# Performance work log

Measured on AMD Instinct MI355X. Metric: run time of the kernel, lower is better.

## Reference

```python
import jax, jax.numpy as jnp
import numpy as np

DIM = 768


def setup_inputs() -> dict:
    key = jax.random.key(0)
    k1, k2, k3, k4, k5 = jax.random.split(key, 5)
    lines = jax.random.normal(k1, (32, 512, DIM), dtype=jnp.float32)
    videos = jax.random.normal(k2, (32, 128, DIM), dtype=jnp.float32)
    video_mask = jax.random.randint(k3, (32, 128), 0, 2, dtype=jnp.int32)
    # nn.Linear(dim, dim, bias=False) weights, applied as x @ W.T
    w_q = jax.random.normal(k4, (DIM, DIM), dtype=jnp.float32) * (DIM ** -0.5)
    w_k = jax.random.normal(k5, (DIM, DIM), dtype=jnp.float32) * (DIM ** -0.5)
    return {"lines": lines, "videos": videos, "video_mask": video_mask, "w_q": w_q, "w_k": w_k}


def reference(lines, videos, video_mask, w_q, w_k):
    scale = DIM ** -0.5
    q = jnp.einsum('bld,ed->ble', lines, w_q)   # (B, L, D)
    k = jnp.einsum('bvd,ed->bve', videos, w_k)  # (B, V, D)
    scores = jnp.einsum('bld,bvd->blv', q, k) * scale
    pad = (video_mask == 0)[:, None, :]          # (B, 1, V)
    scores = jnp.where(pad, jnp.float32(-1e9), scores)
    weights = jax.nn.softmax(scores, axis=-1)    # (B, L, V)
    return jnp.einsum('blv,bvd->bld', weights, videos)
```

## Files before the change

kernel.cpp:

```cpp
#include <hip/hip_runtime.h>

#define DIM 768
#define NB  32
#define LQ  512
#define NV  128

typedef unsigned short u16;
typedef unsigned int   u32;
typedef __bf16 bf16x8 __attribute__((ext_vector_type(8)));
typedef float  f32x4  __attribute__((ext_vector_type(4)));
typedef u16    u16x8  __attribute__((ext_vector_type(8)));
typedef u16    u16x4  __attribute__((ext_vector_type(4)));

typedef __attribute__((address_space(1))) const void gvoid;
typedef __attribute__((address_space(3))) void       svoid;

__device__ __forceinline__ u16 f2bf(float f) {
    u32 u = __float_as_uint(f);
    return (u16)((u + 0x7FFFu + ((u >> 16) & 1u)) >> 16);
}

__device__ __forceinline__ bf16x8 ld_frag(const u16* p) {
    return __builtin_bit_cast(bf16x8, *(const u16x8*)p);
}

__device__ __forceinline__ void gld16(const void* g, void* l) {
    __builtin_amdgcn_global_load_lds((gvoid*)g, (svoid*)l, 16, 0, 0);
}

#define W2S    4
#define W2_BLK (36 * W2S)
#define NL_BLK 6144

__global__ __launch_bounds__(256) void prep_kernel(const float* __restrict__ lines,
                                                   const float* __restrict__ w_q,
                                                   const float* __restrict__ w_k,
                                                   const float* __restrict__ videos,
                                                   u16* __restrict__ lbf,
                                                   float* __restrict__ w2f,
                                                   u16* __restrict__ vt2,
                                                   u16* __restrict__ vbf) {
    __shared__ union {
        u16 T[64][136];
        struct { u16 q[128][72]; u16 k[128][72]; } w2s;
    } uL;
    const int bx = blockIdx.x;
    const int t  = threadIdx.x;

    if (bx < W2_BLK) {
        const int tile = bx / W2S, kc = bx % W2S;
        const int m0 = (tile / 6) * 128;
        const int n0 = (tile % 6) * 128;
        const int w    = t >> 6;
        const int lane = t & 63;
        const int quad = lane >> 4;
        const int ln   = lane & 15;
        const int wr   = (w >> 1) * 64;
        const int wc   = (w & 1) * 64;
        f32x4 acc[4][4] = {};
        for (int ks = kc * 3; ks < kc * 3 + 3; ++ks) {
            __syncthreads();
            const int e0 = ks * 64;
#pragma unroll
            for (int p = 0; p < 8; ++p) {
                int f  = t + p * 256;
                int r  = f >> 5;
                int c4 = f & 31;
                float4 xq = *(const float4*)(w_q + (size_t)(e0 + r) * DIM + m0 + c4 * 4);
                float4 xk = *(const float4*)(w_k + (size_t)(e0 + r) * DIM + n0 + c4 * 4);
                int swz = ((r >> 3) ^ ((c4 >> 1) & 7)) * 8 + (r & 7);
                uL.w2s.q[c4 * 4 + 0][swz] = f2bf(xq.x);
                uL.w2s.q[c4 * 4 + 1][swz] = f2bf(xq.y);
                uL.w2s.q[c4 * 4 + 2][swz] = f2bf(xq.z);
                uL.w2s.q[c4 * 4 + 3][swz] = f2bf(xq.w);
                uL.w2s.k[c4 * 4 + 0][swz] = f2bf(xk.x);
                uL.w2s.k[c4 * 4 + 1][swz] = f2bf(xk.y);
                uL.w2s.k[c4 * 4 + 2][swz] = f2bf(xk.z);
                uL.w2s.k[c4 * 4 + 3][swz] = f2bf(xk.w);
            }
            __syncthreads();
#pragma unroll
            for (int kk = 0; kk < 2; ++kk) {
                bf16x8 af[4], bfr[4];
#pragma unroll
                for (int i = 0; i < 4; ++i) {
                    int row = wr + i * 16 + ln;
                    af[i]  = ld_frag(&uL.w2s.q[row][((kk * 4 + quad) ^ ((row >> 3) & 7)) * 8]);
                }
#pragma unroll
                for (int j = 0; j < 4; ++j) {
                    int row = wc + j * 16 + ln;
                    bfr[j] = ld_frag(&uL.w2s.k[row][((kk * 4 + quad) ^ ((row >> 3) & 7)) * 8]);
                }
#pragma unroll
                for (int i = 0; i < 4; ++i)
#pragma unroll
                    for (int j = 0; j < 4; ++j)
                        acc[i][j] = __builtin_amdgcn_mfma_f32_16x16x32_bf16(af[i], bfr[j], acc[i][j], 0, 0, 0);
            }
        }
#pragma unroll
        for (int i = 0; i < 4; ++i)
#pragma unroll
            for (int j = 0; j < 4; ++j)
#pragma unroll
                for (int r = 0; r < 4; ++r)
                    atomicAdd(&w2f[(size_t)(m0 + wr + i * 16 + quad * 4 + r) * DIM +
                                   n0 + wc + j * 16 + ln], acc[i][j][r]);
        return;
    }

    if (bx < W2_BLK + NL_BLK) {
        size_t i = (size_t)(bx - W2_BLK) * 256 + t;
        float4 a = ((const float4*)lines)[i * 2];
        float4 b = ((const float4*)lines)[i * 2 + 1];
        u16x8 o = { f2bf(a.x), f2bf(a.y), f2bf(a.z), f2bf(a.w),
                    f2bf(b.x), f2bf(b.y), f2bf(b.z), f2bf(b.w) };
        ((u16x8*)lbf)[i] = o;
        return;
    }

    const int v  = bx - (W2_BLK + NL_BLK);
    const int b  = v / 12;
    const int d0 = (v % 12) * 64;
    const float* src = videos + (size_t)b * NV * DIM;
#pragma unroll
    for (int p = 0; p < 8; ++p) {
        int f  = t + p * 256;
        int vv = f >> 4;
        int c4 = f & 15;
        float4 x = *(const float4*)(src + (size_t)vv * DIM + d0 + c4 * 4);
        u16x4 o = { f2bf(x.x), f2bf(x.y), f2bf(x.z), f2bf(x.w) };
        uL.T[c4 * 4 + 0][vv] = o[0];
        uL.T[c4 * 4 + 1][vv] = o[1];
        uL.T[c4 * 4 + 2][vv] = o[2];
        uL.T[c4 * 4 + 3][vv] = o[3];
        *(u16x4*)(vbf + ((size_t)b * NV + vv) * DIM + d0 + c4 * 4) = o;
    }
    __syncthreads();
#pragma unroll
    for (int p = 0; p < 4; ++p) {
        int f  = t + p * 256;
        int dl = f >> 4;
        int v8 = f & 15;
        int d  = d0 + dl;
        int it = d >> 7, wv = (d >> 4) & 7, lnn = d & 15;
        int ks = v8 >> 2, qd = v8 & 3;
        int lane = qd * 16 + lnn;
        size_t off = ((((size_t)b * 6 + it) * 8 + wv) * 4 + ks) * 512 + lane * 8;
        *(u16x8*)(vt2 + off) = *(const u16x8*)&uL.T[dl][v8 * 8];
    }
}

__global__ __launch_bounds__(512) void g_kernel(const u16* __restrict__ A,
                                                const float* __restrict__ Wf,
                                                u16* __restrict__ C) {
    __shared__ u16 sA[128][64];
    __shared__ u16 sB[128][72];
    const int t    = threadIdx.x;
    const int w    = t >> 6;
    const int lane = t & 63;
    const int quad = lane >> 4;
    const int ln   = lane & 15;

    int m0, n0;
    {
        int i = blockIdx.x;
        int xcd = i & 7, s = i >> 3;
        m0 = ((s / 6) * 8 + xcd) * 128;
        n0 = (s % 6) * 128;
    }

    const int wr = (w >> 2) * 64;
    const int wc = (w & 3) * 32;
    const int srow   = lane >> 3;
    const int schunk = (lane & 7) ^ srow;

    f32x4 acc[4][2] = {};
#pragma unroll
    for (int ks = 0; ks < 12; ++ks) {
        __syncthreads();
#pragma unroll
        for (int p = 0; p < 2; ++p) {
            int rb = w * 16 + p * 8;
            gld16(A + (size_t)(m0 + rb + srow) * DIM + ks * 64 + schunk * 8, &sA[rb][0]);
        }
#pragma unroll
        for (int p = 0; p < 4; ++p) {
            int idx = t + p * 512;
            int row = idx >> 4, c4 = idx & 15;
            float4 x = *(const float4*)(Wf + (size_t)(n0 + row) * DIM + ks * 64 + c4 * 4);
            u16x4 o = { f2bf(x.x), f2bf(x.y), f2bf(x.z), f2bf(x.w) };
            int swz = ((c4 >> 1) ^ (row & 7)) * 8 + (c4 & 1) * 4;
            *(u16x4*)&sB[row][swz] = o;
        }
        __syncthreads();
#pragma unroll
        for (int kk = 0; kk < 2; ++kk) {
            bf16x8 af[4], bfr[2];
#pragma unroll
            for (int i = 0; i < 4; ++i)
                af[i]  = ld_frag(&sA[wr + i * 16 + ln][((kk * 4 + quad) ^ (ln & 7)) * 8]);
#pragma unroll
            for (int j = 0; j < 2; ++j)
                bfr[j] = ld_frag(&sB[wc + j * 16 + ln][((kk * 4 + quad) ^ (ln & 7)) * 8]);
#pragma unroll
            for (int i = 0; i < 4; ++i)
#pragma unroll
                for (int j = 0; j < 2; ++j)
                    acc[i][j] = __builtin_amdgcn_mfma_f32_16x16x32_bf16(af[i], bfr[j], acc[i][j], 0, 0, 0);
        }
    }
#pragma unroll
    for (int i = 0; i < 4; ++i)
#pragma unroll
        for (int j = 0; j < 2; ++j)
#pragma unroll
            for (int r = 0; r < 4; ++r)
                C[(size_t)(m0 + wr + i * 16 + quad * 4 + r) * DIM + n0 + wc + j * 16 + ln] =
                    f2bf(acc[i][j][r]);
}

__global__ __launch_bounds__(512) void attn_kernel(const u16* __restrict__ Q,
                                                   const u16* __restrict__ K,
                                                   const u16* __restrict__ Vt2,
                                                   const int* __restrict__ mask,
                                                   float* __restrict__ out) {
    int b, l0;
    {
        int i = blockIdx.x;
        int xcd = i & 7, s = i >> 3;
        b  = (s >> 3) * 8 + xcd;
        l0 = (s & 7) * 64;
    }
    const int t    = threadIdx.x;
    const int w    = t >> 6;
    const int lane = t & 63;
    const int quad = lane >> 4;
    const int ln   = lane & 15;

    __shared__ union {
        struct { u16 q[64][64]; u16 k[128][64]; } st;
        float s[64][132];
    } uA;
    __shared__ union {
        struct { u16 q[64][64]; u16 k[128][64]; } st;
        u16 p[64][136];
    } uB;
    __shared__ float sBias[128];

    const u16* Qb = Q + ((size_t)b * LQ + l0) * DIM;
    const u16* Kb = K + (size_t)b * NV * DIM;
    if (t < NV) sBias[t] = mask[b * NV + t] ? 0.0f : -1e9f;

    const int srow   = lane >> 3;
    const int schunk = (lane & 7) ^ srow;

    auto stage = [&](int ks, int sel) {
        u16 (*q)[64] = sel ? uB.st.q : uA.st.q;
        u16 (*k)[64] = sel ? uB.st.k : uA.st.k;
        gld16(Qb + (size_t)(w * 8 + srow) * DIM + ks * 64 + schunk * 8, &q[w * 8][0]);
        gld16(Kb + (size_t)(w * 16 + srow) * DIM + ks * 64 + schunk * 8, &k[w * 16][0]);
        gld16(Kb + (size_t)(w * 16 + 8 + srow) * DIM + ks * 64 + schunk * 8, &k[w * 16 + 8][0]);
    };

    f32x4 accS[4] = {};
    stage(0, 0);
#pragma unroll
    for (int ks = 0; ks < 12; ++ks) {
        __syncthreads();
        if (ks < 11) stage(ks + 1, (ks + 1) & 1);
        u16 (*q)[64] = (ks & 1) ? uB.st.q : uA.st.q;
        u16 (*k)[64] = (ks & 1) ? uB.st.k : uA.st.k;
#pragma unroll
        for (int kk = 0; kk < 2; ++kk) {
            bf16x8 bfr = ld_frag(&k[w * 16 + ln][((kk * 4 + quad) ^ (ln & 7)) * 8]);
#pragma unroll
            for (int i = 0; i < 4; ++i) {
                bf16x8 af = ld_frag(&q[i * 16 + ln][((kk * 4 + quad) ^ (ln & 7)) * 8]);
                accS[i] = __builtin_amdgcn_mfma_f32_16x16x32_bf16(af, bfr, accS[i], 0, 0, 0);
            }
        }
    }
    __syncthreads();
    const float scale = 0.03608439182435161f;
#pragma unroll
    for (int i = 0; i < 4; ++i)
#pragma unroll
        for (int r = 0; r < 4; ++r)
            uA.s[i * 16 + quad * 4 + r][w * 16 + ln] = accS[i][r] * scale;
    __syncthreads();

    {
        const int row = t >> 3, seg = t & 7;
        float vals[16];
        float mx = -3.0e38f;
#pragma unroll
        for (int c = 0; c < 4; ++c) {
            float4 x  = *(const float4*)&uA.s[row][seg * 16 + c * 4];
            float4 bz = *(const float4*)&sBias[seg * 16 + c * 4];
            float a0 = x.x + bz.x, a1 = x.y + bz.y, a2 = x.z + bz.z, a3 = x.w + bz.w;
            vals[c * 4 + 0] = a0; vals[c * 4 + 1] = a1;
            vals[c * 4 + 2] = a2; vals[c * 4 + 3] = a3;
            mx = fmaxf(mx, fmaxf(fmaxf(a0, a1), fmaxf(a2, a3)));
        }
        mx = fmaxf(mx, __shfl_xor(mx, 1));
        mx = fmaxf(mx, __shfl_xor(mx, 2));
        mx = fmaxf(mx, __shfl_xor(mx, 4));
        float sum = 0.0f;
#pragma unroll
        for (int c = 0; c < 16; ++c) { float e = __expf(vals[c] - mx); vals[c] = e; sum += e; }
        sum += __shfl_xor(sum, 1);
        sum += __shfl_xor(sum, 2);
        sum += __shfl_xor(sum, 4);
        const float inv = 1.0f / sum;
        __syncthreads();
#pragma unroll
        for (int h = 0; h < 2; ++h) {
            u16x8 pk;
#pragma unroll
            for (int e = 0; e < 8; ++e) pk[e] = f2bf(vals[h * 8 + e] * inv);
            *(u16x8*)&uB.p[row][seg * 16 + h * 8] = pk;
        }
    }
    __syncthreads();

    bf16x8 paf[4][4];
#pragma unroll
    for (int i = 0; i < 4; ++i)
#pragma unroll
        for (int ks = 0; ks < 4; ++ks)
            paf[i][ks] = ld_frag(&uB.p[i * 16 + ln][ks * 32 + quad * 8]);

    const u16* V2 = Vt2 + (size_t)b * 6 * 8 * 4 * 512;
    float*     Ob = out + ((size_t)b * LQ + l0) * DIM;
    for (int it = 0; it < 6; ++it) {
        f32x4 accO[4] = {};
#pragma unroll
        for (int ks = 0; ks < 4; ++ks) {
            bf16x8 bv = ld_frag(V2 + (((size_t)(it * 8 + w)) * 4 + ks) * 512 + lane * 8);
#pragma unroll
            for (int i = 0; i < 4; ++i)
                accO[i] = __builtin_amdgcn_mfma_f32_16x16x32_bf16(paf[i][ks], bv, accO[i], 0, 0, 0);
        }
#pragma unroll
        for (int i = 0; i < 4; ++i)
#pragma unroll
            for (int r = 0; r < 4; ++r)
                Ob[(size_t)(i * 16 + quad * 4 + r) * DIM + it * 128 + w * 16 + ln] = accO[i][r];
    }
}

extern "C" void kernel_launch(void* const* d_in, const int* in_sizes, int n_in,
                              void* d_out, int out_size, void* d_ws, size_t ws_size,
                              hipStream_t stream) {
    const float* lines  = (const float*)d_in[0];
    const float* videos = (const float*)d_in[1];
    const int*   mask   = (const int*)d_in[2];
    const float* w_q    = (const float*)d_in[3];
    const float* w_k    = (const float*)d_in[4];
    float*       out    = (float*)d_out;

    u16*   gw  = (u16*)d_ws;
    u16*   vt2 = gw  + (size_t)NB * NV * DIM;
    u16*   lbf = vt2 + (size_t)NB * DIM * NV;
    u16*   vbf = lbf + (size_t)NB * LQ * DIM;
    float* w2f = (float*)(vbf + (size_t)NB * NV * DIM);

    hipMemsetAsync(w2f, 0, (size_t)DIM * DIM * sizeof(float), stream);
    prep_kernel<<<W2_BLK + NL_BLK + 384, 256, 0, stream>>>(
        lines, w_q, w_k, videos, lbf, w2f, vt2, vbf);
    g_kernel   <<<192, 512, 0, stream>>>(vbf, w2f, gw);
    attn_kernel<<<256, 512, 0, stream>>>(lbf, gw, vt2, mask, out);
}
```

Baseline: 165.3 us.

## Fuse lines fp32-to-bf16 conversion into attention kernel Q staging

The separate prep pass that converted `lines` to a bf16 buffer is removed. The attention kernel now loads fp32 Q rows directly into registers, converts them to bf16, and writes them into swizzled, double-buffered LDS while the current stage's MFMAs run. This drops a full write and re-read of a 25 MB intermediate plus 6144 prep blocks. In exchange, Q staging moves from async LDS loads to register loads, which adds VGPR pressure and some latency inside the main loop. It also drops one redundant barrier before the P write.

```diff
diff --git a/kernel.cpp b/kernel.cpp
--- a/kernel.cpp
+++ b/kernel.cpp
@@ -30,13 +30,10 @@
 
 #define W2S    4
 #define W2_BLK (36 * W2S)
-#define NL_BLK 6144
-
-__global__ __launch_bounds__(256) void prep_kernel(const float* __restrict__ lines,
-                                                   const float* __restrict__ w_q,
+
+__global__ __launch_bounds__(256) void prep_kernel(const float* __restrict__ w_q,
                                                    const float* __restrict__ w_k,
                                                    const float* __restrict__ videos,
-                                                   u16* __restrict__ lbf,
                                                    float* __restrict__ w2f,
                                                    u16* __restrict__ vt2,
                                                    u16* __restrict__ vbf) {
@@ -110,17 +107,7 @@
         return;
     }
 
-    if (bx < W2_BLK + NL_BLK) {
-        size_t i = (size_t)(bx - W2_BLK) * 256 + t;
-        float4 a = ((const float4*)lines)[i * 2];
-        float4 b = ((const float4*)lines)[i * 2 + 1];
-        u16x8 o = { f2bf(a.x), f2bf(a.y), f2bf(a.z), f2bf(a.w),
-                    f2bf(b.x), f2bf(b.y), f2bf(b.z), f2bf(b.w) };
-        ((u16x8*)lbf)[i] = o;
-        return;
-    }
-
-    const int v  = bx - (W2_BLK + NL_BLK);
+    const int v  = bx - W2_BLK;
     const int b  = v / 12;
     const int d0 = (v % 12) * 64;
     const float* src = videos + (size_t)b * NV * DIM;
@@ -221,7 +208,7 @@
                     f2bf(acc[i][j][r]);
 }
 
-__global__ __launch_bounds__(512) void attn_kernel(const u16* __restrict__ Q,
+__global__ __launch_bounds__(512) void attn_kernel(const float* __restrict__ Qf,
                                                    const u16* __restrict__ K,
                                                    const u16* __restrict__ Vt2,
                                                    const int* __restrict__ mask,
@@ -240,47 +227,63 @@
     const int ln   = lane & 15;
 
     __shared__ union {
-        struct { u16 q[64][64]; u16 k[128][64]; } st;
+        struct { u16 q[2][64][64]; u16 k[2][128][64]; } st;
         float s[64][132];
     } uA;
-    __shared__ union {
-        struct { u16 q[64][64]; u16 k[128][64]; } st;
-        u16 p[64][136];
-    } uB;
+    __shared__ u16 sP[64][136];
     __shared__ float sBias[128];
 
-    const u16* Qb = Q + ((size_t)b * LQ + l0) * DIM;
-    const u16* Kb = K + (size_t)b * NV * DIM;
+    const float* Qb = Qf + ((size_t)b * LQ + l0) * DIM;
+    const u16*   Kb = K + (size_t)b * NV * DIM;
     if (t < NV) sBias[t] = mask[b * NV + t] ? 0.0f : -1e9f;
 
     const int srow   = lane >> 3;
     const int schunk = (lane & 7) ^ srow;
-
-    auto stage = [&](int ks, int sel) {
-        u16 (*q)[64] = sel ? uB.st.q : uA.st.q;
-        u16 (*k)[64] = sel ? uB.st.k : uA.st.k;
-        gld16(Qb + (size_t)(w * 8 + srow) * DIM + ks * 64 + schunk * 8, &q[w * 8][0]);
-        gld16(Kb + (size_t)(w * 16 + srow) * DIM + ks * 64 + schunk * 8, &k[w * 16][0]);
-        gld16(Kb + (size_t)(w * 16 + 8 + srow) * DIM + ks * 64 + schunk * 8, &k[w * 16 + 8][0]);
+    const int qrow = t >> 3;
+    const int qc8  = t & 7;
+    const int qswz = (qc8 ^ (qrow & 7)) * 8;
+
+    auto stageK = [&](int ks, int sel) {
+        gld16(Kb + (size_t)(w * 16 + srow) * DIM + ks * 64 + schunk * 8, &uA.st.k[sel][w * 16][0]);
+        gld16(Kb + (size_t)(w * 16 + 8 + srow) * DIM + ks * 64 + schunk * 8, &uA.st.k[sel][w * 16 + 8][0]);
     };
+    auto loadQ = [&](int ks, float4& x0, float4& x1) {
+        const float* p = Qb + (size_t)qrow * DIM + ks * 64 + qc8 * 8;
+        x0 = *(const float4*)p;
+        x1 = *(const float4*)(p + 4);
+    };
+    auto writeQ = [&](int sel, const float4& x0, const float4& x1) {
+        u16x8 o = { f2bf(x0.x), f2bf(x0.y), f2bf(x0.z), f2bf(x0.w),
+                    f2bf(x1.x), f2bf(x1.y), f2bf(x1.z), f2bf(x1.w) };
+        *(u16x8*)&uA.st.q[sel][qrow][qswz] = o;
+    };
 
     f32x4 accS[4] = {};
-    stage(0, 0);
+    {
+        float4 x0, x1;
+        loadQ(0, x0, x1);
+        stageK(0, 0);
+        writeQ(0, x0, x1);
+    }
 #pragma unroll
     for (int ks = 0; ks < 12; ++ks) {
         __syncthreads();
-        if (ks < 11) stage(ks + 1, (ks + 1) & 1);
-        u16 (*q)[64] = (ks & 1) ? uB.st.q : uA.st.q;
-        u16 (*k)[64] = (ks & 1) ? uB.st.k : uA.st.k;
+        const int sel = ks & 1;
+        float4 nx0, nx1;
+        if (ks < 11) {
+            loadQ(ks + 1, nx0, nx1);
+            stageK(ks + 1, sel ^ 1);
+        }
 #pragma unroll
         for (int kk = 0; kk < 2; ++kk) {
-            bf16x8 bfr = ld_frag(&k[w * 16 + ln][((kk * 4 + quad) ^ (ln & 7)) * 8]);
+            bf16x8 bfr = ld_frag(&uA.st.k[sel][w * 16 + ln][((kk * 4 + quad) ^ (ln & 7)) * 8]);
 #pragma unroll
             for (int i = 0; i < 4; ++i) {
-                bf16x8 af = ld_frag(&q[i * 16 + ln][((kk * 4 + quad) ^ (ln & 7)) * 8]);
+                bf16x8 af = ld_frag(&uA.st.q[sel][i * 16 + ln][((kk * 4 + quad) ^ (ln & 7)) * 8]);
                 accS[i] = __builtin_amdgcn_mfma_f32_16x16x32_bf16(af, bfr, accS[i], 0, 0, 0);
             }
         }
+        if (ks < 11) writeQ(sel ^ 1, nx0, nx1);
     }
     __syncthreads();
     const float scale = 0.03608439182435161f;
@@ -314,13 +317,12 @@
         sum += __shfl_xor(sum, 2);
         sum += __shfl_xor(sum, 4);
         const float inv = 1.0f / sum;
-        __syncthreads();
 #pragma unroll
         for (int h = 0; h < 2; ++h) {
             u16x8 pk;
 #pragma unroll
             for (int e = 0; e < 8; ++e) pk[e] = f2bf(vals[h * 8 + e] * inv);
-            *(u16x8*)&uB.p[row][seg * 16 + h * 8] = pk;
+            *(u16x8*)&sP[row][seg * 16 + h * 8] = pk;
         }
     }
     __syncthreads();
@@ -330,7 +332,7 @@
     for (int i = 0; i < 4; ++i)
 #pragma unroll
         for (int ks = 0; ks < 4; ++ks)
-            paf[i][ks] = ld_frag(&uB.p[i * 16 + ln][ks * 32 + quad * 8]);
+            paf[i][ks] = ld_frag(&sP[i * 16 + ln][ks * 32 + quad * 8]);
 
     const u16* V2 = Vt2 + (size_t)b * 6 * 8 * 4 * 512;
     float*     Ob = out + ((size_t)b * LQ + l0) * DIM;
@@ -363,13 +365,11 @@
 
     u16*   gw  = (u16*)d_ws;
     u16*   vt2 = gw  + (size_t)NB * NV * DIM;
-    u16*   lbf = vt2 + (size_t)NB * DIM * NV;
-    u16*   vbf = lbf + (size_t)NB * LQ * DIM;
+    u16*   vbf = vt2 + (size_t)NB * DIM * NV;
     float* w2f = (float*)(vbf + (size_t)NB * NV * DIM);
 
     hipMemsetAsync(w2f, 0, (size_t)DIM * DIM * sizeof(float), stream);
-    prep_kernel<<<W2_BLK + NL_BLK + 384, 256, 0, stream>>>(
-        lines, w_q, w_k, videos, lbf, w2f, vt2, vbf);
+    prep_kernel<<<W2_BLK + 384, 256, 0, stream>>>(w_q, w_k, videos, w2f, vt2, vbf);
     g_kernel   <<<192, 512, 0, stream>>>(vbf, w2f, gw);
-    attn_kernel<<<256, 512, 0, stream>>>(lbf, gw, vt2, mask, out);
-}
+    attn_kernel<<<256, 512, 0, stream>>>(lines, gw, vt2, mask, out);
+}
```

New measurement: 165.5 us. Within noise of the previous version (+0.1%).
